# Kernel tuning notes

Measured on AMD Instinct MI355X. Metric: run time of the kernel, lower is better.

The kernel has to match this reference:

```python
import jax, jax.numpy as jnp
import numpy as np

NC, K, SD = 8, 1024, 64
L = NC * SD
B = 8192
TAU = 0.07
COMMIT_W = 1.0
CONTRAST_W = 1.0
EPS = 1e-12


def setup_inputs() -> dict:
    key = jax.random.key(0)
    kz, ke = jax.random.split(key)
    z = jax.random.normal(kz, (B, L), dtype=jnp.float32)
    embeddings = jax.random.normal(ke, (NC, K, SD), dtype=jnp.float32)
    return {"z": z, "embeddings": embeddings}


def reference(z, embeddings):
    sg = jax.lax.stop_gradient
    Bn, Ln = z.shape
    nc, k, sd = embeddings.shape
    zr = z.reshape(Bn, nc, sd)  # (B, nc, sd)

    # squared distances via ||z||^2 - 2 z.e + ||e||^2 -> (B, nc, K), avoids (B,nc,K,sd)
    z2 = jnp.sum(zr * zr, axis=-1)[:, :, None]
    e2 = jnp.sum(embeddings * embeddings, axis=-1)[None, :, :]
    cross = jnp.einsum('bnd,nkd->bnk', zr, embeddings)
    dists = z2 - 2.0 * cross + e2
    indices = jnp.argmin(dists, axis=-1)  # (B, nc)

    # codebook gather
    quant_splits = embeddings[jnp.arange(nc)[None, :], indices]  # (B, nc, sd)
    quant_z = quant_splits.reshape(Bn, Ln)

    commit_loss = jnp.mean((sg(quant_z) - z) ** 2)
    embed_loss = jnp.mean((quant_z - sg(z)) ** 2)
    total_commit = commit_loss + embed_loss

    quant_z_st = z + sg(quant_z - z)

    z_norm = z / jnp.maximum(jnp.linalg.norm(z, axis=-1, keepdims=True), EPS)
    q_det = sg(quant_z)
    q_norm = q_det / jnp.maximum(jnp.linalg.norm(q_det, axis=-1, keepdims=True), EPS)
    logits = jnp.matmul(q_norm, z_norm.T) / TAU  # (B, B)
    # cross-entropy with labels = arange(B)
    contrastive = jnp.mean(jax.nn.logsumexp(logits, axis=1) - jnp.diagonal(logits))

    return (quant_z_st, COMMIT_W * total_commit, CONTRAST_W * contrastive, indices)
```

## Files before the change

kernel.cpp:

```cpp
#include <hip/hip_runtime.h>
#include <cstdint>
#include <cstddef>

#define NCB   8
#define KC    1024
#define SDIM  64
#define LDIM  512
#define BATCH 8192
#define INV_TAU (1.0f/0.07f)
#define K2E  20.60992915555662f
#define STR8 272
#define DBIAS 256.0f

typedef __bf16 bf16_t;
typedef bf16_t bf16x8 __attribute__((ext_vector_type(8)));
typedef float  floatx4 __attribute__((ext_vector_type(4)));
typedef int    intx8  __attribute__((ext_vector_type(8)));

__device__ __forceinline__ unsigned short f2bf(float f) {
    union { float f; unsigned int u; } c; c.f = f;
    unsigned int u = c.u;
    u += 0x7fffu + ((u >> 16) & 1u);
    return (unsigned short)(u >> 16);
}
__device__ __forceinline__ float bf2f(unsigned short h) {
    union { unsigned int u; float f; } c; c.u = ((unsigned int)h) << 16;
    return c.f;
}
__device__ __forceinline__ float exp2_fast(float x) {
    float r; asm("v_exp_f32 %0, %1" : "=v"(r) : "v"(x)); return r;
}

__global__ __launch_bounds__(256) void
k_pre(const float* __restrict__ emb, float* __restrict__ e2,
      unsigned short* __restrict__ eh, unsigned short* __restrict__ el,
      float* __restrict__ accs) {
    int id = blockIdx.x * 256 + threadIdx.x;
    const float4* e4 = (const float4*)(emb + (size_t)id * SDIM);
    ushort4* eh4 = (ushort4*)(eh + (size_t)id * SDIM);
    ushort4* el4 = (ushort4*)(el + (size_t)id * SDIM);
    float s0=0.f,s1=0.f,s2=0.f,s3=0.f;
#pragma unroll
    for (int i=0;i<16;i++){ float4 v=e4[i];
        s0=fmaf(v.x,v.x,s0); s1=fmaf(v.y,v.y,s1);
        s2=fmaf(v.z,v.z,s2); s3=fmaf(v.w,v.w,s3);
        ushort4 h, l;
        h.x=f2bf(v.x); l.x=f2bf(v.x-bf2f(h.x));
        h.y=f2bf(v.y); l.y=f2bf(v.y-bf2f(h.y));
        h.z=f2bf(v.z); l.z=f2bf(v.z-bf2f(h.z));
        h.w=f2bf(v.w); l.w=f2bf(v.w-bf2f(h.w));
        eh4[i]=h; el4[i]=l;
    }
    e2[id] = (s0+s1)+(s2+s3);
    if (id==0){ accs[0]=0.f; accs[1]=0.f; accs[2]=0.f; }
}

__device__ __forceinline__ double dist64d(const float* __restrict__ e,
                                          const float* __restrict__ zg) {
    double se=0.0, sz=0.0;
#pragma unroll 8
    for (int i=0;i<64;i++){ double ev=(double)e[i];
        se = fma(ev,ev,se); sz = fma(ev,(double)zg[i],sz); }
    return se - 2.0*sz;
}

__global__ __launch_bounds__(256,2) void
k_argmin(const unsigned short* __restrict__ eh, const unsigned short* __restrict__ el,
         const float* __restrict__ e2, const float* __restrict__ z,
         const float* __restrict__ emb, float* __restrict__ out_q,
         float* __restrict__ out_idx, float* __restrict__ accs) {
    __shared__ unsigned short Ah[128*72], Al[128*72];
    __shared__ unsigned short Bh[128*72], Bl[128*72];
    __shared__ float e2s[128];
    __shared__ unsigned int mK[2][128][2];

    const int tid = threadIdx.x;
    const int n   = blockIdx.y;
    const int i0  = blockIdx.x * 128;
    const int wid = tid >> 6, lane = tid & 63;
    const int wm = wid & 1, wn = wid >> 1;
    const int c  = lane & 15, qq = lane >> 4;

#pragma unroll
    for (int s=0;s<8;s++){
        int seg = tid + s*256;
        int r = seg >> 4, sg = seg & 15;
        float4 v = *(const float4*)(z + (size_t)(i0+r)*LDIM + n*SDIM + sg*4);
        ushort4 h, l;
        h.x=f2bf(v.x); l.x=f2bf(v.x-bf2f(h.x));
        h.y=f2bf(v.y); l.y=f2bf(v.y-bf2f(h.y));
        h.z=f2bf(v.z); l.z=f2bf(v.z-bf2f(h.z));
        h.w=f2bf(v.w); l.w=f2bf(v.w-bf2f(h.w));
        *(ushort4*)(&Ah[r*72+sg*4]) = h;
        *(ushort4*)(&Al[r*72+sg*4]) = l;
    }

    unsigned int k1[16], k2[16];
#pragma unroll
    for (int j=0;j<16;j++){ k1[j]=0xFFFFFFFFu; k2[j]=0xFFFFFFFFu; }

    const unsigned short* ehn = eh + (size_t)n*KC*SDIM;
    const unsigned short* eln = el + (size_t)n*KC*SDIM;
    const float* e2n = e2 + n*KC;

    for (int jt=0; jt<8; jt++){
        const int j0 = jt*128;
        __syncthreads();
#pragma unroll
        for (int s=0;s<4;s++){
            int seg = tid + s*256; int r = seg>>3, sg = seg&7;
            size_t go = (size_t)(j0+r)*SDIM + sg*8;
            *(uint4*)(&Bh[r*72+sg*8]) = *(const uint4*)(ehn + go);
            *(uint4*)(&Bl[r*72+sg*8]) = *(const uint4*)(eln + go);
        }
        if (tid < 128) e2s[tid] = e2n[j0+tid] + DBIAS;
        __syncthreads();

        floatx4 acc[4][4];
#pragma unroll
        for (int mt=0;mt<4;mt++)
#pragma unroll
            for (int nt=0;nt<4;nt++) acc[mt][nt] = (floatx4){0.f,0.f,0.f,0.f};

#pragma unroll
        for (int t=0;t<2;t++){
            bf16x8 ah[4], al[4], bh[4], bl[4];
#pragma unroll
            for (int mt=0;mt<4;mt++){
                ah[mt] = *(const bf16x8*)(&Ah[(wm*64+mt*16+c)*72 + t*32 + qq*8]);
                al[mt] = *(const bf16x8*)(&Al[(wm*64+mt*16+c)*72 + t*32 + qq*8]);
            }
#pragma unroll
            for (int nt=0;nt<4;nt++){
                bh[nt] = *(const bf16x8*)(&Bh[(wn*64+nt*16+c)*72 + t*32 + qq*8]);
                bl[nt] = *(const bf16x8*)(&Bl[(wn*64+nt*16+c)*72 + t*32 + qq*8]);
            }
#pragma unroll
            for (int mt=0;mt<4;mt++)
#pragma unroll
                for (int nt=0;nt<4;nt++){
                    acc[mt][nt] = __builtin_amdgcn_mfma_f32_16x16x32_bf16(ah[mt], bh[nt], acc[mt][nt], 0,0,0);
                    acc[mt][nt] = __builtin_amdgcn_mfma_f32_16x16x32_bf16(ah[mt], bl[nt], acc[mt][nt], 0,0,0);
                    acc[mt][nt] = __builtin_amdgcn_mfma_f32_16x16x32_bf16(al[mt], bh[nt], acc[mt][nt], 0,0,0);
                }
        }

#pragma unroll
        for (int nt=0;nt<4;nt++){
            const int colb = wn*64 + nt*16 + c;
            float e2v = e2s[colb];
            unsigned int kidx = (unsigned int)(j0 + colb);
#pragma unroll
            for (int mt=0;mt<4;mt++)
#pragma unroll
                for (int reg=0;reg<4;reg++){
                    float d = fmaf(-2.0f, acc[mt][nt][reg], e2v);
                    unsigned int key = (__float_as_uint(d) & 0xFFFFFC00u) | kidx;
                    int s = mt*4+reg;
                    unsigned int o1 = k1[s];
                    k2[s] = min(k2[s], max(key, o1));
                    k1[s] = min(o1, key);
                }
        }
    }

#pragma unroll
    for (int off=1; off<16; off<<=1){
#pragma unroll
        for (int s=0;s<16;s++){
            unsigned int o1 = __shfl_xor(k1[s], off);
            unsigned int o2 = __shfl_xor(k2[s], off);
            unsigned int n1 = min(k1[s], o1);
            k2[s] = min( max(k1[s], o1), min(k2[s], o2) );
            k1[s] = n1;
        }
    }
    if (c == 0){
#pragma unroll
        for (int s=0;s<16;s++){
            int row = wm*64 + (s>>2)*16 + qq*4 + (s&3);
            mK[wn][row][0] = k1[s]; mK[wn][row][1] = k2[s];
        }
    }
    __syncthreads();

    if (tid < 128){
        int b = i0 + tid;
        unsigned int a1 = mK[0][tid][0], a2 = mK[0][tid][1];
        unsigned int c1 = mK[1][tid][0], c2 = mK[1][tid][1];
        unsigned int f1 = min(a1, c1);
        unsigned int f2 = min( max(a1, c1), min(a2, c2) );
        int ii1 = (int)(f1 & 0x3FFu);
        int ii2 = (int)(f2 & 0x3FFu);
        float d1q = __uint_as_float(f1 & 0xFFFFFC00u);
        float d2q = __uint_as_float(f2 & 0xFFFFFC00u);

        const float* eb = emb + (size_t)n*KC*SDIM;
        const float* zg = z + (size_t)b*LDIM + n*SDIM;
        if (d2q - d1q < 0.08f) {
            double d1 = dist64d(eb + (size_t)ii1*SDIM, zg);
            double d2 = dist64d(eb + (size_t)ii2*SDIM, zg);
            if (d2 < d1 || (d2 == d1 && ii2 < ii1)) ii1 = ii2;
        }

        const float4* q4 = (const float4*)(eb + (size_t)ii1*SDIM);
        const float4* z4 = (const float4*)zg;
        float4* oq = (float4*)(out_q + (size_t)b*LDIM + n*SDIM);
        float cs = 0.f;
#pragma unroll
        for (int i=0;i<16;i++){
            float4 v = q4[i]; float4 zv = z4[i];
            oq[i] = v;
            float d0=v.x-zv.x, d1=v.y-zv.y, d2=v.z-zv.z, d3=v.w-zv.w;
            cs += d0*d0 + d1*d1 + d2*d2 + d3*d3;
        }
        out_idx[b*NCB + n] = (float)ii1;

        for (int off=32; off; off>>=1) cs += __shfl_down(cs, off);
        if ((tid & 63)==0) atomicAdd(&accs[0], cs);
    }
}

__global__ __launch_bounds__(256) void
k_norm(const float* __restrict__ z, const float* __restrict__ q,
       unsigned char* __restrict__ zn8, unsigned char* __restrict__ qn8,
       float* __restrict__ diag) {
    const int b = blockIdx.x, tid = threadIdx.x;
    const size_t base = (size_t)b*LDIM;
    float2 zv = ((const float2*)(z+base))[tid];
    float2 qv = ((const float2*)(q+base))[tid];
    float sz = zv.x*zv.x + zv.y*zv.y;
    float sq = qv.x*qv.x + qv.y*qv.y;
    float sqz= qv.x*zv.x + qv.y*zv.y;
    for (int off=32; off; off>>=1){
        sz+=__shfl_down(sz,off); sq+=__shfl_down(sq,off); sqz+=__shfl_down(sqz,off);
    }
    __shared__ float red[3][4];
    __shared__ float bc[2];
    int w = tid>>6;
    if ((tid&63)==0){ red[0][w]=sz; red[1][w]=sq; red[2][w]=sqz; }
    __syncthreads();
    if (tid==0){
        float tz = red[0][0]+red[0][1]+red[0][2]+red[0][3];
        float tq = red[1][0]+red[1][1]+red[1][2]+red[1][3];
        float tz_q = red[2][0]+red[2][1]+red[2][2]+red[2][3];
        float inz = 1.0f/fmaxf(sqrtf(tz), 1e-12f);
        float inq = 1.0f/fmaxf(sqrtf(tq), 1e-12f);
        bc[0]=inz; bc[1]=inq;
        diag[b] = tz_q*inz*inq*INV_TAU;
    }
    __syncthreads();
    float inz=bc[0], inq=bc[1];
    int pz = __builtin_amdgcn_cvt_pk_fp8_f32(zv.x*inz, zv.y*inz, 0, false);
    int pq = __builtin_amdgcn_cvt_pk_fp8_f32(qv.x*inq, qv.y*inq, 0, false);
    ((unsigned short*)(zn8+base))[tid] = (unsigned short)(pz & 0xffff);
    ((unsigned short*)(qn8+base))[tid] = (unsigned short)(pq & 0xffff);
}

__global__ __launch_bounds__(256,2) void
k_logits(const unsigned char* __restrict__ qn8, const unsigned char* __restrict__ zn8,
         float* __restrict__ Spart) {
    __shared__ unsigned char As[128*STR8];
    __shared__ unsigned char Bs[128*STR8];
    const int tid  = threadIdx.x;
    const int i0   = blockIdx.x * 128;
    const int chnk = blockIdx.y;
    const int wid  = tid >> 6, lane = tid & 63;
    const int wm = wid & 1, wn = wid >> 1;
    const int c  = lane & 15, qq = lane >> 4;

    float S[16];
#pragma unroll
    for (int i=0;i<16;i++) S[i] = 0.f;

    for (int jt=0;jt<8;jt++){
        const int j0 = chnk*1024 + jt*128;
        floatx4 acc[4][4];
#pragma unroll
        for (int mt=0;mt<4;mt++)
#pragma unroll
            for (int nt=0;nt<4;nt++) acc[mt][nt] = (floatx4){0.f,0.f,0.f,0.f};

        for (int kk=0;kk<512;kk+=256){
            __syncthreads();
#pragma unroll
            for (int s=0;s<8;s++){
                int seg = tid + s*256;
                int r = seg >> 4, sg = seg & 15;
                *(uint4*)(&As[r*STR8 + sg*16]) =
                    *(const uint4*)(qn8 + (size_t)(i0+r)*LDIM + kk + sg*16);
            }
#pragma unroll
            for (int s=0;s<8;s++){
                int seg = tid + s*256;
                int r = seg >> 4, sg = seg & 15;
                *(uint4*)(&Bs[r*STR8 + sg*16]) =
                    *(const uint4*)(zn8 + (size_t)(j0+r)*LDIM + kk + sg*16);
            }
            __syncthreads();
#pragma unroll
            for (int t=0;t<2;t++){
                intx8 af[4], bfr[4];
#pragma unroll
                for (int mt=0;mt<4;mt++){
                    const unsigned char* p = &As[(wm*64+mt*16+c)*STR8 + t*128 + qq*32];
                    union { intx8 v; uint4 h[2]; } u;
                    u.h[0] = *(const uint4*)(p);
                    u.h[1] = *(const uint4*)(p+16);
                    af[mt] = u.v;
                }
#pragma unroll
                for (int nt=0;nt<4;nt++){
                    const unsigned char* p = &Bs[(wn*64+nt*16+c)*STR8 + t*128 + qq*32];
                    union { intx8 v; uint4 h[2]; } u;
                    u.h[0] = *(const uint4*)(p);
                    u.h[1] = *(const uint4*)(p+16);
                    bfr[nt] = u.v;
                }
#pragma unroll
                for (int mt=0;mt<4;mt++)
#pragma unroll
                    for (int nt=0;nt<4;nt++)
                        acc[mt][nt] = __builtin_amdgcn_mfma_scale_f32_16x16x128_f8f6f4(
                            af[mt], bfr[nt], acc[mt][nt],
                            0, 0,
                            0, 127,
                            0, 127);
            }
        }

#pragma unroll
        for (int mt=0;mt<4;mt++)
#pragma unroll
            for (int reg=0;reg<4;reg++){
                float e0 = exp2_fast(fmaf(acc[mt][0][reg], K2E, -K2E));
                float e1 = exp2_fast(fmaf(acc[mt][1][reg], K2E, -K2E));
                float e2v= exp2_fast(fmaf(acc[mt][2][reg], K2E, -K2E));
                float e3 = exp2_fast(fmaf(acc[mt][3][reg], K2E, -K2E));
                S[mt*4+reg] += (e0+e1)+(e2v+e3);
            }
    }

#pragma unroll
    for (int off=1; off<16; off<<=1)
#pragma unroll
        for (int s=0;s<16;s++) S[s] += __shfl_xor(S[s], off);

    if (c == 0){
        const int p = chnk*2 + wn;
#pragma unroll
        for (int mt=0;mt<4;mt++)
#pragma unroll
            for (int reg=0;reg<4;reg++){
                int row = i0 + wm*64 + mt*16 + qq*4 + reg;
                Spart[p*BATCH + row] = S[mt*4+reg];
            }
    }
}

__global__ __launch_bounds__(256) void
k_finalize(const float* __restrict__ Spart, const float* __restrict__ diag,
           float* __restrict__ accs, float* __restrict__ out_s) {
    int r = blockIdx.x*256 + threadIdx.x;
    float Ssum = 0.f;
#pragma unroll
    for (int p=0;p<16;p++) Ssum += Spart[p*BATCH + r];
    float val = INV_TAU + logf(Ssum) - diag[r];
    for (int off=32; off; off>>=1) val += __shfl_down(val, off);
    if ((threadIdx.x & 63)==0) atomicAdd(&accs[1], val);
    __syncthreads();
    if (threadIdx.x == 0){
        __threadfence();
        unsigned int old = __float_as_uint(atomicAdd(&accs[2], 1.0f));
        if (old == __float_as_uint(31.0f)) {
            __threadfence();
            float a0 = atomicAdd(&accs[0], 0.0f);
            float a1 = atomicAdd(&accs[1], 0.0f);
            out_s[0] = 2.0f*a0 / (float)((size_t)BATCH*LDIM);
            out_s[1] = a1 / (float)BATCH;
        }
    }
}

extern "C" void kernel_launch(void* const* d_in, const int* in_sizes, int n_in,
                              void* d_out, int out_size, void* d_ws, size_t ws_size,
                              hipStream_t stream) {
    const float* z   = (const float*)d_in[0];
    const float* emb = (const float*)d_in[1];
    float* out = (float*)d_out;
    float* out_q       = out;
    float* out_scalars = out + 4194304;
    float* out_idx     = out + 4194306;

    float* wsf   = (float*)d_ws;
    float* e2    = wsf;
    float* accs  = wsf + 8192;
    float* diag  = wsf + 8704;
    float* Spart = wsf + 16896;
    unsigned char* qn8 = (unsigned char*)(Spart + 32*BATCH);
    unsigned char* zn8 = qn8 + (size_t)BATCH*LDIM;
    unsigned short* eh = (unsigned short*)(zn8 + (size_t)BATCH*LDIM);
    unsigned short* el = eh + (size_t)NCB*KC*SDIM;

    k_pre    <<<32,          256, 0, stream>>>(emb, e2, eh, el, accs);
    k_argmin <<<dim3(64,8),  256, 0, stream>>>(eh, el, e2, z, emb,
                                               out_q, out_idx, accs);
    k_norm   <<<BATCH,       256, 0, stream>>>(z, out_q, zn8, qn8, diag);
    k_logits <<<dim3(64,8),  256, 0, stream>>>(qn8, zn8, Spart);
    k_finalize<<<32,         256, 0, stream>>>(Spart, diag, accs, out_scalars);
}
```

Before: 172.2 us.

## Double-buffer B tiles via direct global-to-LDS loads with XOR swizzle in both GEMMs

Both the argmin and the logits kernels now stage their B tiles into double-buffered LDS with global_load_lds, so the next tile's load overlaps the current MFMA work and one barrier per step is removed. The padded LDS strides are replaced by XOR swizzles to avoid bank conflicts. In the logits kernel the A fragments are kept in registers for the whole K dimension instead of being reloaded through LDS, and the N tile is halved to 64. The argmin top-2 update is also merged into a single v_med3 instruction. The trade-offs are higher register pressure from the resident A fragments and more loop iterations with smaller tiles.

```diff
diff --git a/kernel.cpp b/kernel.cpp
--- a/kernel.cpp
+++ b/kernel.cpp
@@ -9,13 +9,13 @@
 #define BATCH 8192
 #define INV_TAU (1.0f/0.07f)
 #define K2E  20.60992915555662f
-#define STR8 272
 #define DBIAS 256.0f
 
 typedef __bf16 bf16_t;
 typedef bf16_t bf16x8 __attribute__((ext_vector_type(8)));
 typedef float  floatx4 __attribute__((ext_vector_type(4)));
 typedef int    intx8  __attribute__((ext_vector_type(8)));
+typedef unsigned int u32;
 
 __device__ __forceinline__ unsigned short f2bf(float f) {
     union { float f; unsigned int u; } c; c.f = f;
@@ -29,6 +29,12 @@
 }
 __device__ __forceinline__ float exp2_fast(float x) {
     float r; asm("v_exp_f32 %0, %1" : "=v"(r) : "v"(x)); return r;
+}
+__device__ __forceinline__ void gll16(const void* g, void* l) {
+    __builtin_amdgcn_global_load_lds(
+        (const __attribute__((address_space(1))) u32*)g,
+        (__attribute__((address_space(3))) u32*)l,
+        16, 0, 0);
 }
 
 __global__ __launch_bounds__(256) void
@@ -69,9 +75,9 @@
          const float* __restrict__ e2, const float* __restrict__ z,
          const float* __restrict__ emb, float* __restrict__ out_q,
          float* __restrict__ out_idx, float* __restrict__ accs) {
-    __shared__ unsigned short Ah[128*72], Al[128*72];
-    __shared__ unsigned short Bh[128*72], Bl[128*72];
-    __shared__ float e2s[128];
+    __shared__ __align__(16) unsigned short Ah[128*64], Al[128*64];
+    __shared__ __align__(16) unsigned short Bh[2][64*64], Bl[2][64*64];
+    __shared__ float e2s[2][64];
     __shared__ unsigned int mK[2][128][2];
 
     const int tid = threadIdx.x;
@@ -91,64 +97,83 @@
         h.y=f2bf(v.y); l.y=f2bf(v.y-bf2f(h.y));
         h.z=f2bf(v.z); l.z=f2bf(v.z-bf2f(h.z));
         h.w=f2bf(v.w); l.w=f2bf(v.w-bf2f(h.w));
-        *(ushort4*)(&Ah[r*72+sg*4]) = h;
-        *(ushort4*)(&Al[r*72+sg*4]) = l;
-    }
+        int off = r*64 + ((sg*4) ^ ((r&7)<<3));
+        *(ushort4*)(&Ah[off]) = h;
+        *(ushort4*)(&Al[off]) = l;
+    }
+
+    const unsigned char* ehb = (const unsigned char*)(eh + (size_t)n*KC*SDIM);
+    const unsigned char* elb = (const unsigned char*)(el + (size_t)n*KC*SDIM);
+    const float* e2n = e2 + n*KC;
+
+    const int brow = lane >> 3;
+    const int bchk = ((lane & 7)*16) ^ (brow << 4);
+
+    auto stageB = [&](int buf, int j0){
+#pragma unroll
+        for (int s=0;s<2;s++){
+            int r0 = wid*16 + s*8;
+            size_t go = (size_t)(j0 + r0 + brow)*128 + bchk;
+            gll16(ehb + go, &Bh[buf][r0*64]);
+            gll16(elb + go, &Bl[buf][r0*64]);
+        }
+    };
+
+    if (tid < 64) e2s[0][tid] = e2n[tid] + DBIAS;
+    stageB(0, 0);
 
     unsigned int k1[16], k2[16];
 #pragma unroll
     for (int j=0;j<16;j++){ k1[j]=0xFFFFFFFFu; k2[j]=0xFFFFFFFFu; }
 
-    const unsigned short* ehn = eh + (size_t)n*KC*SDIM;
-    const unsigned short* eln = el + (size_t)n*KC*SDIM;
-    const float* e2n = e2 + n*KC;
-
-    for (int jt=0; jt<8; jt++){
-        const int j0 = jt*128;
-        __syncthreads();
-#pragma unroll
-        for (int s=0;s<4;s++){
-            int seg = tid + s*256; int r = seg>>3, sg = seg&7;
-            size_t go = (size_t)(j0+r)*SDIM + sg*8;
-            *(uint4*)(&Bh[r*72+sg*8]) = *(const uint4*)(ehn + go);
-            *(uint4*)(&Bl[r*72+sg*8]) = *(const uint4*)(eln + go);
-        }
-        if (tid < 128) e2s[tid] = e2n[j0+tid] + DBIAS;
-        __syncthreads();
-
-        floatx4 acc[4][4];
-#pragma unroll
-        for (int mt=0;mt<4;mt++)
-#pragma unroll
-            for (int nt=0;nt<4;nt++) acc[mt][nt] = (floatx4){0.f,0.f,0.f,0.f};
+    __syncthreads();
+
+    for (int jt=0; jt<16; jt++){
+        const int cur = jt & 1, nxt = cur ^ 1;
+        const int j0 = jt*64;
+        float e2r = 0.f;
+        if (jt < 15){
+            stageB(nxt, j0 + 64);
+            if (tid < 64) e2r = e2n[j0 + 64 + tid];
+        }
+
+        floatx4 acc[4][2];
+#pragma unroll
+        for (int mt=0;mt<4;mt++){
+            acc[mt][0]=(floatx4){0.f,0.f,0.f,0.f};
+            acc[mt][1]=(floatx4){0.f,0.f,0.f,0.f};
+        }
 
 #pragma unroll
         for (int t=0;t<2;t++){
-            bf16x8 ah[4], al[4], bh[4], bl[4];
+            const int axo = (t*32 + qq*8) ^ ((c&7)<<3);
+            bf16x8 ah[4], alo[4], bh[2], bl[2];
 #pragma unroll
             for (int mt=0;mt<4;mt++){
-                ah[mt] = *(const bf16x8*)(&Ah[(wm*64+mt*16+c)*72 + t*32 + qq*8]);
-                al[mt] = *(const bf16x8*)(&Al[(wm*64+mt*16+c)*72 + t*32 + qq*8]);
+                int ro = (wm*64 + mt*16 + c)*64 + axo;
+                ah[mt]  = *(const bf16x8*)(&Ah[ro]);
+                alo[mt] = *(const bf16x8*)(&Al[ro]);
             }
 #pragma unroll
-            for (int nt=0;nt<4;nt++){
-                bh[nt] = *(const bf16x8*)(&Bh[(wn*64+nt*16+c)*72 + t*32 + qq*8]);
-                bl[nt] = *(const bf16x8*)(&Bl[(wn*64+nt*16+c)*72 + t*32 + qq*8]);
+            for (int nt=0;nt<2;nt++){
+                int ro = (wn*32 + nt*16 + c)*64 + axo;
+                bh[nt] = *(const bf16x8*)(&Bh[cur][ro]);
+                bl[nt] = *(const bf16x8*)(&Bl[cur][ro]);
             }
 #pragma unroll
             for (int mt=0;mt<4;mt++)
 #pragma unroll
-                for (int nt=0;nt<4;nt++){
-                    acc[mt][nt] = __builtin_amdgcn_mfma_f32_16x16x32_bf16(ah[mt], bh[nt], acc[mt][nt], 0,0,0);
-                    acc[mt][nt] = __builtin_amdgcn_mfma_f32_16x16x32_bf16(ah[mt], bl[nt], acc[mt][nt], 0,0,0);
-                    acc[mt][nt] = __builtin_amdgcn_mfma_f32_16x16x32_bf16(al[mt], bh[nt], acc[mt][nt], 0,0,0);
+                for (int nt=0;nt<2;nt++){
+                    acc[mt][nt] = __builtin_amdgcn_mfma_f32_16x16x32_bf16(ah[mt],  bh[nt], acc[mt][nt], 0,0,0);
+                    acc[mt][nt] = __builtin_amdgcn_mfma_f32_16x16x32_bf16(ah[mt],  bl[nt], acc[mt][nt], 0,0,0);
+                    acc[mt][nt] = __builtin_amdgcn_mfma_f32_16x16x32_bf16(alo[mt], bh[nt], acc[mt][nt], 0,0,0);
                 }
         }
 
 #pragma unroll
-        for (int nt=0;nt<4;nt++){
-            const int colb = wn*64 + nt*16 + c;
-            float e2v = e2s[colb];
+        for (int nt=0;nt<2;nt++){
+            const int colb = wn*32 + nt*16 + c;
+            float e2v = e2s[cur][colb];
             unsigned int kidx = (unsigned int)(j0 + colb);
 #pragma unroll
             for (int mt=0;mt<4;mt++)
@@ -157,11 +182,16 @@
                     float d = fmaf(-2.0f, acc[mt][nt][reg], e2v);
                     unsigned int key = (__float_as_uint(d) & 0xFFFFFC00u) | kidx;
                     int s = mt*4+reg;
-                    unsigned int o1 = k1[s];
-                    k2[s] = min(k2[s], max(key, o1));
+                    unsigned int o1 = k1[s], o2 = k2[s];
+                    unsigned int nk2;
+                    asm("v_med3_u32 %0, %1, %2, %3" : "=v"(nk2) : "v"(o1), "v"(o2), "v"(key));
+                    k2[s] = nk2;
                     k1[s] = min(o1, key);
                 }
         }
+
+        if (jt < 15 && tid < 64) e2s[nxt][tid] = e2r + DBIAS;
+        __syncthreads();
     }
 
 #pragma unroll
@@ -260,8 +290,7 @@
 __global__ __launch_bounds__(256,2) void
 k_logits(const unsigned char* __restrict__ qn8, const unsigned char* __restrict__ zn8,
          float* __restrict__ Spart) {
-    __shared__ unsigned char As[128*STR8];
-    __shared__ unsigned char Bs[128*STR8];
+    __shared__ __align__(16) unsigned char Bs[2][64*512];
     const int tid  = threadIdx.x;
     const int i0   = blockIdx.x * 128;
     const int chnk = blockIdx.y;
@@ -269,64 +298,73 @@
     const int wm = wid & 1, wn = wid >> 1;
     const int c  = lane & 15, qq = lane >> 4;
 
+    intx8 af[4][4];
+#pragma unroll
+    for (int mt=0;mt<4;mt++){
+        const unsigned char* ap = qn8 + (size_t)(i0 + wm*64 + mt*16 + c)*LDIM + qq*32;
+#pragma unroll
+        for (int kc=0;kc<4;kc++){
+            union { intx8 v; uint4 h[2]; } u;
+            u.h[0] = *(const uint4*)(ap + kc*128);
+            u.h[1] = *(const uint4*)(ap + kc*128 + 16);
+            af[mt][kc] = u.v;
+        }
+    }
+
+    const int brow  = lane >> 5;
+    const int bchk0 = (lane & 31) * 16;
+
+    auto stageB = [&](int buf, int j0){
+#pragma unroll
+        for (int s=0;s<8;s++){
+            int r0  = wid*16 + s*2;
+            int row = r0 + brow;
+            gll16(zn8 + (size_t)(j0+row)*LDIM + (bchk0 ^ ((row&7)<<4)),
+                  &Bs[buf][r0*512]);
+        }
+    };
+
     float S[16];
 #pragma unroll
     for (int i=0;i<16;i++) S[i] = 0.f;
 
-    for (int jt=0;jt<8;jt++){
-        const int j0 = chnk*1024 + jt*128;
-        floatx4 acc[4][4];
-#pragma unroll
-        for (int mt=0;mt<4;mt++)
-#pragma unroll
-            for (int nt=0;nt<4;nt++) acc[mt][nt] = (floatx4){0.f,0.f,0.f,0.f};
-
-        for (int kk=0;kk<512;kk+=256){
-            __syncthreads();
-#pragma unroll
-            for (int s=0;s<8;s++){
-                int seg = tid + s*256;
-                int r = seg >> 4, sg = seg & 15;
-                *(uint4*)(&As[r*STR8 + sg*16]) =
-                    *(const uint4*)(qn8 + (size_t)(i0+r)*LDIM + kk + sg*16);
+    stageB(0, chnk*1024);
+    __syncthreads();
+
+    for (int jt=0;jt<16;jt++){
+        const int cur = jt & 1;
+        const int j0 = chnk*1024 + jt*64;
+        if (jt < 15) stageB(cur^1, j0 + 64);
+
+        floatx4 acc[4][2];
+#pragma unroll
+        for (int mt=0;mt<4;mt++){
+            acc[mt][0]=(floatx4){0.f,0.f,0.f,0.f};
+            acc[mt][1]=(floatx4){0.f,0.f,0.f,0.f};
+        }
+
+#pragma unroll
+        for (int kc=0;kc<4;kc++){
+            intx8 bfr[2];
+#pragma unroll
+            for (int nt=0;nt<2;nt++){
+                const unsigned char* p = &Bs[cur][(wn*32 + nt*16 + c)*512];
+                const int o = kc*128 + qq*32;
+                const int x = (c&7)<<4;
+                union { intx8 v; uint4 h[2]; } u;
+                u.h[0] = *(const uint4*)(p + (o ^ x));
+                u.h[1] = *(const uint4*)(p + ((o + 16) ^ x));
+                bfr[nt] = u.v;
             }
 #pragma unroll
-            for (int s=0;s<8;s++){
-                int seg = tid + s*256;
-                int r = seg >> 4, sg = seg & 15;
-                *(uint4*)(&Bs[r*STR8 + sg*16]) =
-                    *(const uint4*)(zn8 + (size_t)(j0+r)*LDIM + kk + sg*16);
-            }
-            __syncthreads();
-#pragma unroll
-            for (int t=0;t<2;t++){
-                intx8 af[4], bfr[4];
-#pragma unroll
-                for (int mt=0;mt<4;mt++){
-                    const unsigned char* p = &As[(wm*64+mt*16+c)*STR8 + t*128 + qq*32];
-                    union { intx8 v; uint4 h[2]; } u;
-                    u.h[0] = *(const uint4*)(p);
-                    u.h[1] = *(const uint4*)(p+16);
-                    af[mt] = u.v;
-                }
-#pragma unroll
-                for (int nt=0;nt<4;nt++){
-                    const unsigned char* p = &Bs[(wn*64+nt*16+c)*STR8 + t*128 + qq*32];
-                    union { intx8 v; uint4 h[2]; } u;
-                    u.h[0] = *(const uint4*)(p);
-                    u.h[1] = *(const uint4*)(p+16);
-                    bfr[nt] = u.v;
-                }
-#pragma unroll
-                for (int mt=0;mt<4;mt++)
-#pragma unroll
-                    for (int nt=0;nt<4;nt++)
-                        acc[mt][nt] = __builtin_amdgcn_mfma_scale_f32_16x16x128_f8f6f4(
-                            af[mt], bfr[nt], acc[mt][nt],
-                            0, 0,
-                            0, 127,
-                            0, 127);
-            }
+            for (int mt=0;mt<4;mt++)
+#pragma unroll
+                for (int nt=0;nt<2;nt++)
+                    acc[mt][nt] = __builtin_amdgcn_mfma_scale_f32_16x16x128_f8f6f4(
+                        af[mt][kc], bfr[nt], acc[mt][nt],
+                        0, 0,
+                        0, 127,
+                        0, 127);
         }
 
 #pragma unroll
@@ -335,10 +373,9 @@
             for (int reg=0;reg<4;reg++){
                 float e0 = exp2_fast(fmaf(acc[mt][0][reg], K2E, -K2E));
                 float e1 = exp2_fast(fmaf(acc[mt][1][reg], K2E, -K2E));
-                float e2v= exp2_fast(fmaf(acc[mt][2][reg], K2E, -K2E));
-                float e3 = exp2_fast(fmaf(acc[mt][3][reg], K2E, -K2E));
-                S[mt*4+reg] += (e0+e1)+(e2v+e3);
+                S[mt*4+reg] += e0 + e1;
             }
+        __syncthreads();
     }
 
 #pragma unroll
```

Result: no change. 169.9 us (-1.3%).
